# Optimization experiments

Measured on AMD Instinct MI355X. Metric: run time of the kernel, lower is better.

Reference implementation:

```python
import jax, jax.numpy as jnp
import numpy as np

B, C, H, W = 8, 256, 128, 128
EPS = 1e-12  # F.normalize eps


def setup_inputs() -> dict:
    key = jax.random.key(0)
    k0, k1, k2, k3 = jax.random.split(key, 4)
    x = jax.random.normal(k0, (B, C, H, W), jnp.float32)
    # qkv: Conv2d(C, 3C, 1, bias=False) -> weight [3C, C]
    w_qkv = jax.random.normal(k1, (3 * C, C), jnp.float32) * 0.02
    # qkv_dwconv: Conv2d(3C, 3C, 1, groups=3C) -> per-channel scale [3C]
    w_dw = jax.random.normal(k2, (3 * C,), jnp.float32) * 0.1 + 1.0
    # temperature: Parameter(ones(num_heads=1, 1, 1))
    temperature = jnp.ones((1, 1, 1), jnp.float32)
    # project_out: Conv2d(C, C, 1, bias=False) -> weight [C, C]
    w_proj = jax.random.normal(k3, (C, C), jnp.float32) * 0.02
    return {"x": x, "w_qkv": w_qkv, "w_dw": w_dw,
            "temperature": temperature, "w_proj": w_proj}


def reference(x, w_qkv, w_dw, temperature, w_proj):
    b, c, h, w = x.shape
    n = h * w
    # pointwise conv + depthwise 1x1 conv (= per-channel scale)
    qkv = jnp.einsum('bchw,oc->bohw', x, w_qkv) * w_dw[None, :, None, None]
    q, k, v = jnp.split(qkv, 3, axis=1)          # each [b, c, h, w]
    q = q.reshape(b, c, n)
    k = k.reshape(b, c, n)
    v = v.reshape(b, c, n)
    # L2-normalize along spatial dim (F.normalize: x / max(||x||, eps))
    q = q / jnp.maximum(jnp.linalg.norm(q, axis=-1, keepdims=True), EPS)
    k = k / jnp.maximum(jnp.linalg.norm(k, axis=-1, keepdims=True), EPS)
    # channel-wise cosine attention: [b, c, c]
    attn = jnp.einsum('bcn,bdn->bcd', q, k) * temperature[0]
    attn = jax.nn.softmax(attn, axis=-1)
    out = jnp.einsum('bcd,bdn->bcn', attn, v).reshape(b, c, h, w)
    out = jnp.einsum('bchw,oc->bohw', out, w_proj)
    return out
```

## Files before the change

### kernel.cpp

```cpp
#include <hip/hip_runtime.h>
#include <hip/hip_bf16.h>
#include <stdint.h>

#define NB 8
#define NC 256
#define NN 16384
#define KS 64

typedef short bf16x8 __attribute__((ext_vector_type(8)));
typedef float f32x4  __attribute__((ext_vector_type(4)));
typedef uint32_t u32;

__device__ __forceinline__ unsigned short f2bf(float f) {
  union { float f; unsigned u; } c; c.f = f;
  return (unsigned short)((c.u + 0x7FFFu + ((c.u >> 16) & 1u)) >> 16);
}
__device__ __forceinline__ float bf2f(unsigned short h) {
  union { unsigned u; float f; } c; c.u = ((unsigned)h) << 16;
  return c.f;
}
__device__ __forceinline__ u32 pk2(float a, float b) {
  union { __hip_bfloat162 h; u32 u; } c;
  c.h = __float22bfloat162_rn(make_float2(a, b));
  return c.u;
}

__device__ __forceinline__ void gload16(const void* g, void* l) {
  __builtin_amdgcn_global_load_lds(
      (const __attribute__((address_space(1))) u32*)g,
      (__attribute__((address_space(3))) u32*)l, 16, 0, 0);
}

__device__ __forceinline__ void stage_tile(const char* src, int ld_bytes,
                                           char* lds, int w, int l) {
#pragma unroll
  for (int i = 0; i < 4; ++i) {
    int s = (w * 4 + i) * 64 + l;
    int row = s >> 3;
    int srcslot = (l & 7) ^ (row & 7);
    gload16(src + (size_t)row * ld_bytes + srcslot * 16,
            lds + (w * 4 + i) * 1024);
  }
}

__global__ __launch_bounds__(1024) void k_gramT(
    const float* __restrict__ x, unsigned short* __restrict__ gpart,
    char* __restrict__ xt,
    const float* __restrict__ wqkv, const float* __restrict__ wdw,
    float* __restrict__ Wcat, float* __restrict__ WkT,
    float* __restrict__ Wv2) {
  __shared__ __align__(16) unsigned short tile[256 * 72];
  const int bid = blockIdx.x;
  const int tid = threadIdx.x;

  if (bid >= KS * NB) {
    const int r = (bid - KS * NB) * 4 + (tid >> 8);
    const int t = tid & 255;
    Wcat[r * 256 + t] = wqkv[r * 256 + t] * wdw[r];
    float kv = wqkv[(256 + r) * 256 + t] * wdw[256 + r];
    Wcat[65536 + r * 256 + t] = kv;
    WkT[t * 256 + r] = kv;
    Wv2[r * 256 + t] = wqkv[(512 + r) * 256 + t] * wdw[512 + r];
    return;
  }

  const int ks = bid & (KS - 1), b = bid >> 6;
  const int w = tid >> 6, l = tid & 63;
  const int wm = w >> 2, wn = w & 3;
  const int cg = tid >> 4, ng = tid & 15;
  const int c0 = cg * 4, n0 = ng * 4;
  f32x4 acc[4][4];
#pragma unroll
  for (int m = 0; m < 4; ++m)
#pragma unroll
    for (int n = 0; n < 4; ++n) acc[m][n] = (f32x4){0.f, 0.f, 0.f, 0.f};
  const float* x0 = x + (size_t)b * NC * NN + (size_t)ks * 256;

  float4 f[4];
  u32 hw[4][2];

#define LOADS(kt)                                                           \
  {                                                                         \
    _Pragma("unroll") for (int j = 0; j < 4; ++j)                           \
        f[j] = *(const float4*)&x0[(size_t)(c0 + j) * NN + (kt) * 64 + n0]; \
  }
#define CVT()                                                               \
  {                                                                         \
    _Pragma("unroll") for (int j = 0; j < 4; ++j) {                         \
      hw[j][0] = pk2(f[j].x, f[j].y);                                       \
      hw[j][1] = pk2(f[j].z, f[j].w);                                       \
    }                                                                       \
  }
#define DSW()                                                               \
  {                                                                         \
    _Pragma("unroll") for (int j = 0; j < 4; ++j)                           \
        *(uint2*)&tile[(c0 + j) * 72 + n0] = make_uint2(hw[j][0], hw[j][1]);\
  }

  LOADS(0); CVT(); DSW();
  __syncthreads();

  for (int kt = 0; kt < 4; ++kt) {
    if (kt < 3) LOADS(kt + 1);
#pragma unroll
    for (int ks2 = 0; ks2 < 2; ++ks2) {
      const int ko = ks2 * 32 + (l >> 4) * 8;
      bf16x8 av[4], bv[4];
#pragma unroll
      for (int m = 0; m < 4; ++m) {
        int row = wm * 64 + m * 16 + (l & 15);
        av[m] = *(const bf16x8*)&tile[row * 72 + ko];
      }
#pragma unroll
      for (int n = 0; n < 4; ++n) {
        int row = wn * 64 + n * 16 + (l & 15);
        bv[n] = *(const bf16x8*)&tile[row * 72 + ko];
      }
#pragma unroll
      for (int m = 0; m < 4; ++m)
#pragma unroll
        for (int n = 0; n < 4; ++n)
          acc[m][n] = __builtin_amdgcn_mfma_f32_16x16x32_bf16(
              av[m], bv[n], acc[m][n], 0, 0, 0);
    }
    {
      const int gn = ks * 256 + kt * 64 + n0;
#pragma unroll
      for (int k = 0; k < 4; ++k) {
        u32 e0 = (k < 2) ? (hw[0][0] >> (16 * k)) : (hw[0][1] >> (16 * (k - 2)));
        u32 e1 = (k < 2) ? (hw[1][0] >> (16 * k)) : (hw[1][1] >> (16 * (k - 2)));
        u32 e2 = (k < 2) ? (hw[2][0] >> (16 * k)) : (hw[2][1] >> (16 * (k - 2)));
        u32 e3 = (k < 2) ? (hw[3][0] >> (16 * k)) : (hw[3][1] >> (16 * (k - 2)));
        uint2 ov = make_uint2((e0 & 0xffff) | (e1 << 16),
                              (e2 & 0xffff) | (e3 << 16));
        *(uint2*)(xt + (((size_t)b * NN + gn + k) * 256 + c0) * 2) = ov;
      }
    }
    __syncthreads();
    if (kt < 3) {
      CVT();
      DSW();
      __syncthreads();
    }
  }
#undef LOADS
#undef CVT
#undef DSW
  unsigned short* gp = gpart + ((size_t)(ks * NB + b)) * 65536;
#pragma unroll
  for (int m = 0; m < 4; ++m)
#pragma unroll
    for (int n = 0; n < 4; ++n)
#pragma unroll
      for (int r = 0; r < 4; ++r) {
        int c = wm * 64 + m * 16 + ((l >> 4) << 2) + r;
        int d = wn * 64 + n * 16 + (l & 15);
        gp[(size_t)c * 256 + d] = f2bf(acc[m][n][r]);
      }
}

__global__ __launch_bounds__(256) void k_reduceG(
    const unsigned short* __restrict__ gpart, float* __restrict__ G) {
  const int t = threadIdx.x;
  const int c = blockIdx.x * 2 + (t >> 7), b = blockIdx.y;
  const int d0 = (t & 127) * 2;
  float s0 = 0.f, s1 = 0.f;
#pragma unroll 8
  for (int ks = 0; ks < KS; ++ks) {
    u32 v = *(const u32*)(gpart + (((size_t)ks * NB + b) * 256 + c) * 256 + d0);
    s0 += bf2f((unsigned short)(v & 0xffff));
    s1 += bf2f((unsigned short)(v >> 16));
  }
  *(float2*)(G + ((size_t)b * 256 + c) * 256 + d0) = make_float2(s0, s1);
}

__global__ __launch_bounds__(256) void k_sgT(const float* __restrict__ Wcat,
                                             const float* __restrict__ G,
                                             float* __restrict__ T12,
                                             float* __restrict__ nqk) {
  const int t = threadIdx.x;
  const int r0 = blockIdx.x * 8, b = blockIdx.y;
  const float* Gb = G + (size_t)b * 65536 + t;
  float acc[8] = {0, 0, 0, 0, 0, 0, 0, 0};
#pragma unroll 4
  for (int k = 0; k < 256; ++k) {
    float bv = Gb[(size_t)k * 256];
#pragma unroll
    for (int o = 0; o < 8; ++o) acc[o] += Wcat[(r0 + o) * 256 + k] * bv;
  }
#pragma unroll
  for (int o = 0; o < 8; ++o)
    T12[(size_t)b * 131072 + (size_t)(r0 + o) * 256 + t] = acc[o];
  __shared__ float red[8][4];
  const int w = t >> 6, l = t & 63;
#pragma unroll
  for (int o = 0; o < 8; ++o) {
    float s = acc[o] * Wcat[(r0 + o) * 256 + t];
#pragma unroll
    for (int off = 32; off; off >>= 1) s += __shfl_xor(s, off);
    if (l == 0) red[o][w] = s;
  }
  __syncthreads();
  if (t < 8)
    nqk[b * 512 + r0 + t] = red[t][0] + red[t][1] + red[t][2] + red[t][3];
}

__global__ __launch_bounds__(256) void k_ssoft(const float* __restrict__ T12,
                                               const float* __restrict__ WkT,
                                               const float* __restrict__ nqk,
                                               const float* __restrict__ temp,
                                               float* __restrict__ attn) {
  const int t = threadIdx.x;
  const int c0 = blockIdx.x * 8, b = blockIdx.y;
  const float* Ab = T12 + (size_t)b * 131072 + (size_t)c0 * 256;
  const float* Bb = WkT + t;
  float acc[8] = {0, 0, 0, 0, 0, 0, 0, 0};
#pragma unroll 4
  for (int k = 0; k < 256; ++k) {
    float bv = Bb[(size_t)k * 256];
#pragma unroll
    for (int o = 0; o < 8; ++o) acc[o] += Ab[o * 256 + k] * bv;
  }
  const float rk = 1.0f / fmaxf(sqrtf(fmaxf(nqk[b * 512 + 256 + t], 0.f)), 1e-12f);
  const float tau = temp[0];
#pragma unroll
  for (int o = 0; o < 8; ++o) {
    float rq = 1.0f / fmaxf(sqrtf(fmaxf(nqk[b * 512 + c0 + o], 0.f)), 1e-12f);
    acc[o] = acc[o] * rq * rk * tau;
  }
  __shared__ float redm[8][4];
  __shared__ float reds[8][4];
  const int w = t >> 6, l = t & 63;
#pragma unroll
  for (int o = 0; o < 8; ++o) {
    float m = acc[o];
#pragma unroll
    for (int off = 32; off; off >>= 1) m = fmaxf(m, __shfl_xor(m, off));
    if (l == 0) redm[o][w] = m;
  }
  __syncthreads();
  float e[8];
#pragma unroll
  for (int o = 0; o < 8; ++o) {
    float m = fmaxf(fmaxf(redm[o][0], redm[o][1]), fmaxf(redm[o][2], redm[o][3]));
    e[o] = __expf(acc[o] - m);
    float s = e[o];
#pragma unroll
    for (int off = 32; off; off >>= 1) s += __shfl_xor(s, off);
    if (l == 0) reds[o][w] = s;
  }
  __syncthreads();
#pragma unroll
  for (int o = 0; o < 8; ++o) {
    float tot = reds[o][0] + reds[o][1] + reds[o][2] + reds[o][3];
    attn[(size_t)b * 65536 + (size_t)(c0 + o) * 256 + t] = e[o] / tot;
  }
}

__global__ __launch_bounds__(256) void k_sg2x(const float* __restrict__ wp,
                                              const float* __restrict__ attn,
                                              const float* __restrict__ wv2,
                                              char* __restrict__ Fb) {
  __shared__ float P[8 * 256];
  const int t = threadIdx.x;
  const int o0 = blockIdx.x * 8, b = blockIdx.y;
  const float* Ab = wp + (size_t)o0 * 256;
  const float* Bb = attn + (size_t)b * 65536 + t;
  float acc[8] = {0, 0, 0, 0, 0, 0, 0, 0};
#pragma unroll 4
  for (int k = 0; k < 256; ++k) {
    float bv = Bb[(size_t)k * 256];
#pragma unroll
    for (int o = 0; o < 8; ++o) acc[o] += Ab[o * 256 + k] * bv;
  }
#pragma unroll
  for (int o = 0; o < 8; ++o) P[o * 256 + t] = acc[o];
  __syncthreads();
  float a2[8] = {0, 0, 0, 0, 0, 0, 0, 0};
  const float* Bv = wv2 + t;
#pragma unroll 4
  for (int k = 0; k < 256; ++k) {
    float bv = Bv[(size_t)k * 256];
#pragma unroll
    for (int o = 0; o < 8; ++o) a2[o] += P[o * 256 + k] * bv;
  }
  unsigned short* Cp = (unsigned short*)Fb + (size_t)b * 65536;
#pragma unroll
  for (int o = 0; o < 8; ++o) Cp[(size_t)(o0 + o) * 256 + t] = f2bf(a2[o]);
}

__global__ __launch_bounds__(256) void k_final(const char* __restrict__ xt,
                                               const char* __restrict__ fb,
                                               float* __restrict__ out) {
  __shared__ char smem[32768];
  const int tid = threadIdx.x;
  const int nt = blockIdx.x, ot = blockIdx.y, b = blockIdx.z;
  const int w = tid >> 6, l = tid & 63;
  const int wm = w >> 1, wn = w & 1;
  f32x4 acc[4][4];
#pragma unroll
  for (int m = 0; m < 4; ++m)
#pragma unroll
    for (int nq = 0; nq < 4; ++nq) acc[m][nq] = (f32x4){0.f, 0.f, 0.f, 0.f};
  const char* Ap = xt + ((size_t)b * NN + (size_t)nt * 128) * 512;
  const char* Bp = fb + ((size_t)(b * 256 + ot * 128)) * 512;

  for (int kt = 0; kt < 4; ++kt) {
    stage_tile(Ap + kt * 128, 512, smem, w, l);
    stage_tile(Bp + kt * 128, 512, smem + 16384, w, l);
    __syncthreads();
#pragma unroll
    for (int ks = 0; ks < 2; ++ks) {
      bf16x8 av[4], bv[4];
      const int kb = ks * 64 + ((l >> 4) << 4);
#pragma unroll
      for (int m = 0; m < 4; ++m) {
        int row = wm * 64 + m * 16 + (l & 15);
        av[m] = *(const bf16x8*)(smem + row * 128 + (kb ^ ((row & 7) << 4)));
      }
#pragma unroll
      for (int nq = 0; nq < 4; ++nq) {
        int row = wn * 64 + nq * 16 + (l & 15);
        bv[nq] = *(const bf16x8*)(smem + 16384 + row * 128 +
                                  (kb ^ ((row & 7) << 4)));
      }
#pragma unroll
      for (int m = 0; m < 4; ++m)
#pragma unroll
        for (int nq = 0; nq < 4; ++nq)
          acc[m][nq] = __builtin_amdgcn_mfma_f32_16x16x32_bf16(
              av[m], bv[nq], acc[m][nq], 0, 0, 0);
    }
    __syncthreads();
  }
#pragma unroll
  for (int m = 0; m < 4; ++m)
#pragma unroll
    for (int nq = 0; nq < 4; ++nq) {
      int o = ot * 128 + wn * 64 + nq * 16 + (l & 15);
      int n = nt * 128 + wm * 64 + m * 16 + ((l >> 4) << 2);
      *(f32x4*)(out + ((size_t)(b * 256 + o)) * NN + n) = acc[m][nq];
    }
}

extern "C" void kernel_launch(void* const* d_in, const int* in_sizes, int n_in,
                              void* d_out, int out_size, void* d_ws, size_t ws_size,
                              hipStream_t stream) {
  const float* x     = (const float*)d_in[0];
  const float* wqkv  = (const float*)d_in[1];
  const float* wdwf  = (const float*)d_in[2];
  const float* temp  = (const float*)d_in[3];
  const float* wproj = (const float*)d_in[4];
  float* out = (float*)d_out;
  char* ws = (char*)d_ws;

  char*  xt    = ws;
  unsigned short* gpart = (unsigned short*)(ws + 67108864);
  float* G     = (float*)(ws + 134217728);
  float* T12   = (float*)(ws + 136314880);
  float* attn  = (float*)(ws + 140509184);
  char*  Fb    = ws + 142606336;
  float* Wcat  = (float*)(ws + 143654912);
  float* WkT   = (float*)(ws + 144179200);
  float* Wv2   = (float*)(ws + 144441344);
  float* nqk   = (float*)(ws + 144703488);

  k_gramT<<<dim3(KS * NB + 64), dim3(1024), 0, stream>>>(
      x, gpart, xt, wqkv, wdwf, Wcat, WkT, Wv2);
  k_reduceG<<<dim3(128, NB), dim3(256), 0, stream>>>(gpart, G);
  k_sgT<<<dim3(64, NB), dim3(256), 0, stream>>>(Wcat, G, T12, nqk);
  k_ssoft<<<dim3(32, NB), dim3(256), 0, stream>>>(T12, WkT, nqk, temp, attn);
  k_sg2x<<<dim3(32, NB), dim3(256), 0, stream>>>(wproj, attn, Wv2, Fb);
  k_final<<<dim3(128, 2, NB), dim3(256), 0, stream>>>(xt, Fb, out);
}
```

Measured before the change: 233.6 us.

## Drop transposed bf16 x copy; final GEMM reads fp32 x and transposes in LDS

The Gram kernel no longer writes a transposed bf16 copy of x to workspace. The final projection GEMM instead loads fp32 x directly, converts it to bf16 and transposes it into a padded LDS tile. The split-K factor of the Gram kernel is halved, which shrinks the partial-Gram buffer and the reduce traffic but gives each block twice the K work. The trade is removing one 64MB write and its bf16 reads, in exchange for reading fp32 x twice (once per output-channel tile) and adding conversion and LDS transpose work in the final kernel.

```diff
diff --git a/kernel.cpp b/kernel.cpp
--- a/kernel.cpp
+++ b/kernel.cpp
@@ -5,7 +5,7 @@
 #define NB 8
 #define NC 256
 #define NN 16384
-#define KS 64
+#define KS 32
 
 typedef short bf16x8 __attribute__((ext_vector_type(8)));
 typedef float f32x4  __attribute__((ext_vector_type(4)));
@@ -45,7 +45,6 @@
 
 __global__ __launch_bounds__(1024) void k_gramT(
     const float* __restrict__ x, unsigned short* __restrict__ gpart,
-    char* __restrict__ xt,
     const float* __restrict__ wqkv, const float* __restrict__ wdw,
     float* __restrict__ Wcat, float* __restrict__ WkT,
     float* __restrict__ Wv2) {
@@ -64,17 +63,16 @@
     return;
   }
 
-  const int ks = bid & (KS - 1), b = bid >> 6;
+  const int ks = bid & (KS - 1), b = bid >> 5;
   const int w = tid >> 6, l = tid & 63;
   const int wm = w >> 2, wn = w & 3;
-  const int cg = tid >> 4, ng = tid & 15;
-  const int c0 = cg * 4, n0 = ng * 4;
+  const int c0 = (tid >> 4) * 4, n0 = (tid & 15) * 4;
   f32x4 acc[4][4];
 #pragma unroll
   for (int m = 0; m < 4; ++m)
 #pragma unroll
     for (int n = 0; n < 4; ++n) acc[m][n] = (f32x4){0.f, 0.f, 0.f, 0.f};
-  const float* x0 = x + (size_t)b * NC * NN + (size_t)ks * 256;
+  const float* x0 = x + (size_t)b * NC * NN + (size_t)ks * 512;
 
   float4 f[4];
   u32 hw[4][2];
@@ -100,8 +98,8 @@
   LOADS(0); CVT(); DSW();
   __syncthreads();
 
-  for (int kt = 0; kt < 4; ++kt) {
-    if (kt < 3) LOADS(kt + 1);
+  for (int kt = 0; kt < 8; ++kt) {
+    if (kt < 7) LOADS(kt + 1);
 #pragma unroll
     for (int ks2 = 0; ks2 < 2; ++ks2) {
       const int ko = ks2 * 32 + (l >> 4) * 8;
@@ -123,21 +121,8 @@
           acc[m][n] = __builtin_amdgcn_mfma_f32_16x16x32_bf16(
               av[m], bv[n], acc[m][n], 0, 0, 0);
     }
-    {
-      const int gn = ks * 256 + kt * 64 + n0;
-#pragma unroll
-      for (int k = 0; k < 4; ++k) {
-        u32 e0 = (k < 2) ? (hw[0][0] >> (16 * k)) : (hw[0][1] >> (16 * (k - 2)));
-        u32 e1 = (k < 2) ? (hw[1][0] >> (16 * k)) : (hw[1][1] >> (16 * (k - 2)));
-        u32 e2 = (k < 2) ? (hw[2][0] >> (16 * k)) : (hw[2][1] >> (16 * (k - 2)));
-        u32 e3 = (k < 2) ? (hw[3][0] >> (16 * k)) : (hw[3][1] >> (16 * (k - 2)));
-        uint2 ov = make_uint2((e0 & 0xffff) | (e1 << 16),
-                              (e2 & 0xffff) | (e3 << 16));
-        *(uint2*)(xt + (((size_t)b * NN + gn + k) * 256 + c0) * 2) = ov;
-      }
-    }
     __syncthreads();
-    if (kt < 3) {
+    if (kt < 7) {
       CVT();
       DSW();
       __syncthreads();
@@ -289,40 +274,55 @@
   for (int o = 0; o < 8; ++o) Cp[(size_t)(o0 + o) * 256 + t] = f2bf(a2[o]);
 }
 
-__global__ __launch_bounds__(256) void k_final(const char* __restrict__ xt,
+__global__ __launch_bounds__(256) void k_final(const float* __restrict__ x,
                                                const char* __restrict__ fb,
                                                float* __restrict__ out) {
-  __shared__ char smem[32768];
+  __shared__ __align__(16) unsigned short At[128 * 72];
+  __shared__ __align__(16) char Bs[16384];
   const int tid = threadIdx.x;
   const int nt = blockIdx.x, ot = blockIdx.y, b = blockIdx.z;
   const int w = tid >> 6, l = tid & 63;
   const int wm = w >> 1, wn = w & 1;
+  const int c0 = (tid & 7) * 8, n0 = (tid >> 3) * 4;
   f32x4 acc[4][4];
 #pragma unroll
   for (int m = 0; m < 4; ++m)
 #pragma unroll
     for (int nq = 0; nq < 4; ++nq) acc[m][nq] = (f32x4){0.f, 0.f, 0.f, 0.f};
-  const char* Ap = xt + ((size_t)b * NN + (size_t)nt * 128) * 512;
+  const float* xb = x + (size_t)b * NC * NN + (size_t)nt * 128;
   const char* Bp = fb + ((size_t)(b * 256 + ot * 128)) * 512;
 
   for (int kt = 0; kt < 4; ++kt) {
-    stage_tile(Ap + kt * 128, 512, smem, w, l);
-    stage_tile(Bp + kt * 128, 512, smem + 16384, w, l);
+    stage_tile(Bp + kt * 128, 512, Bs, w, l);
+#pragma unroll
+    for (int g = 0; g < 2; ++g) {
+      float4 f[4];
+#pragma unroll
+      for (int j = 0; j < 4; ++j)
+        f[j] = *(const float4*)&xb[(size_t)(kt * 64 + c0 + g * 4 + j) * NN + n0];
+#pragma unroll
+      for (int k = 0; k < 4; ++k) {
+        float v0 = ((const float*)&f[0])[k], v1 = ((const float*)&f[1])[k];
+        float v2 = ((const float*)&f[2])[k], v3 = ((const float*)&f[3])[k];
+        *(uint2*)&At[(n0 + k) * 72 + c0 + g * 4] =
+            make_uint2(pk2(v0, v1), pk2(v2, v3));
+      }
+    }
     __syncthreads();
 #pragma unroll
     for (int ks = 0; ks < 2; ++ks) {
+      const int kb = ks * 64 + ((l >> 4) << 4);
+      const int ko = ks * 32 + ((l >> 4) << 3);
       bf16x8 av[4], bv[4];
-      const int kb = ks * 64 + ((l >> 4) << 4);
 #pragma unroll
       for (int m = 0; m < 4; ++m) {
         int row = wm * 64 + m * 16 + (l & 15);
-        av[m] = *(const bf16x8*)(smem + row * 128 + (kb ^ ((row & 7) << 4)));
+        av[m] = *(const bf16x8*)&At[row * 72 + ko];
       }
 #pragma unroll
       for (int nq = 0; nq < 4; ++nq) {
         int row = wn * 64 + nq * 16 + (l & 15);
-        bv[nq] = *(const bf16x8*)(smem + 16384 + row * 128 +
-                                  (kb ^ ((row & 7) << 4)));
+        bv[nq] = *(const bf16x8*)(Bs + row * 128 + (kb ^ ((row & 7) << 4)));
       }
 #pragma unroll
       for (int m = 0; m < 4; ++m)
@@ -354,22 +354,21 @@
   float* out = (float*)d_out;
   char* ws = (char*)d_ws;
 
-  char*  xt    = ws;
-  unsigned short* gpart = (unsigned short*)(ws + 67108864);
-  float* G     = (float*)(ws + 134217728);
-  float* T12   = (float*)(ws + 136314880);
-  float* attn  = (float*)(ws + 140509184);
-  char*  Fb    = ws + 142606336;
-  float* Wcat  = (float*)(ws + 143654912);
-  float* WkT   = (float*)(ws + 144179200);
-  float* Wv2   = (float*)(ws + 144441344);
-  float* nqk   = (float*)(ws + 144703488);
+  unsigned short* gpart = (unsigned short*)ws;
+  float* G     = (float*)(ws + 33554432);
+  float* T12   = (float*)(ws + 35651584);
+  float* attn  = (float*)(ws + 39845888);
+  char*  Fb    = ws + 41943040;
+  float* Wcat  = (float*)(ws + 42991616);
+  float* WkT   = (float*)(ws + 43515904);
+  float* Wv2   = (float*)(ws + 43778048);
+  float* nqk   = (float*)(ws + 44040192);
 
   k_gramT<<<dim3(KS * NB + 64), dim3(1024), 0, stream>>>(
-      x, gpart, xt, wqkv, wdwf, Wcat, WkT, Wv2);
+      x, gpart, wqkv, wdwf, Wcat, WkT, Wv2);
   k_reduceG<<<dim3(128, NB), dim3(256), 0, stream>>>(gpart, G);
   k_sgT<<<dim3(64, NB), dim3(256), 0, stream>>>(Wcat, G, T12, nqk);
   k_ssoft<<<dim3(32, NB), dim3(256), 0, stream>>>(T12, WkT, nqk, temp, attn);
   k_sg2x<<<dim3(32, NB), dim3(256), 0, stream>>>(wproj, attn, Wv2, Fb);
-  k_final<<<dim3(128, 2, NB), dim3(256), 0, stream>>>(xt, Fb, out);
-}
+  k_final<<<dim3(128, 2, NB), dim3(256), 0, stream>>>(x, Fb, out);
+}
```

After: 203.9 us. 12.7% less time.
